# Optimization experiments

Measured on AMD Instinct MI355X. Metric: run time of the kernel, lower is better.

The kernel has to match this reference:

```python
import jax, jax.numpy as jnp
import numpy as np

N_CTX = 10  # conv_concat is 10*idf -> idf, so the module expects exactly 10 contexts


def setup_inputs() -> dict:
    key = jax.random.key(0)
    ks = jax.random.split(key, 7)
    B, idf, ih, iw = 32, 256, 32, 32
    cdf, L = 512, 128
    inp = {
        "input": jax.random.normal(ks[0], (B, idf, ih, iw), jnp.float32),
        "contexts": jax.random.normal(ks[1], (N_CTX, B, cdf, L), jnp.float32),
        "Wc": jax.random.normal(ks[2], (idf, cdf), jnp.float32) * 0.02,      # conv_context 1x1, no bias
        "Wcat": jax.random.normal(ks[3], (idf, N_CTX * idf), jnp.float32) * 0.02,  # conv_concat 1x1, no bias
        "Wb": jax.random.normal(ks[4], (idf,), jnp.float32) * 0.02,          # conv_b weight applied to ones -> bias
        "gamma": jnp.ones((idf,), jnp.float32),
        "beta": jnp.zeros((idf,), jnp.float32),
    }
    return inp


def reference(input, contexts, Wc, Wcat, Wb, gamma, beta):
    B, idf, ih, iw = input.shape
    Q = ih * iw
    # target: [B, Q, idf]
    targetT = jnp.transpose(input.reshape(B, idf, Q), (0, 2, 1))
    # project all 10 contexts at once: conv1x1(cdf->idf) == matmul over channel dim
    sourceT = jnp.einsum('dc,nbcl->nbdl', Wc, contexts)          # [N, B, idf, L]
    # attention weights: bmm(targetT, sourceT) then softmax over source dim
    w = jax.nn.softmax(jnp.einsum('bqd,nbdl->nbql', targetT, sourceT), axis=-1)  # [N,B,Q,L]
    attn = jnp.einsum('nbql,nbdl->nbqd', w, sourceT)             # [N, B, Q, idf]
    # torch.cat over last dim in loop order i=0..9 -> interleave as [B,Q,N*idf]
    cat = jnp.transpose(attn, (1, 2, 0, 3)).reshape(B, Q, N_CTX * idf)
    # conv_concat (1x1) over channels + conv_b(ones) bias
    x = jnp.einsum('ef,bqf->bqe', Wcat, cat) + Wb                # [B, Q, idf]
    x = jax.nn.relu(x) + targetT
    # LayerNorm over idf, eps=0, affine
    mu = jnp.mean(x, axis=-1, keepdims=True)
    var = jnp.mean(jnp.square(x - mu), axis=-1, keepdims=True)
    return (x - mu) / jnp.sqrt(var) * gamma + beta
```

## Files before the change

### kernel.cpp

```cpp
#include <hip/hip_runtime.h>
#include <cstdint>

typedef unsigned short u16;
typedef unsigned int   u32;
typedef __bf16 bf16x8 __attribute__((ext_vector_type(8)));
typedef float  f32x4  __attribute__((ext_vector_type(4)));

#define NCTX 10
#define BSZ  32
#define IDF  256
#define QSZ  1024
#define CDF  512
#define LSZ  128

__device__ __forceinline__ u16 f2bf(float f) {
    u32 u = __float_as_uint(f);
    u += 0x7FFFu + ((u >> 16) & 1u);
    return (u16)(u >> 16);
}
__device__ __forceinline__ float bf2f(u16 h) {
    return __uint_as_float(((u32)h) << 16);
}

union U4V { uint4 u; bf16x8 v; };

__device__ __forceinline__ bf16x8 ldg16(const u16* p) {
    U4V t; t.u = *(const uint4*)p; return t.v;
}
__device__ __forceinline__ bf16x8 lds16(const u16* p) {
    U4V t; t.u = *(const uint4*)p; return t.v;
}
__device__ __forceinline__ bf16x8 pack8(const float* f) {
    U4V t;
    t.u.x = (u32)f2bf(f[0]) | ((u32)f2bf(f[1]) << 16);
    t.u.y = (u32)f2bf(f[2]) | ((u32)f2bf(f[3]) << 16);
    t.u.z = (u32)f2bf(f[4]) | ((u32)f2bf(f[5]) << 16);
    t.u.w = (u32)f2bf(f[6]) | ((u32)f2bf(f[7]) << 16);
    return t.v;
}
__device__ __forceinline__ f32x4 mfma16(bf16x8 a, bf16x8 b, f32x4 c) {
    return __builtin_amdgcn_mfma_f32_16x16x32_bf16(a, b, c, 0, 0, 0);
}

__device__ __forceinline__ void gl_lds16(const u16* g, u16* l) {
    __builtin_amdgcn_global_load_lds(
        (__attribute__((address_space(1))) void*)(g),
        (__attribute__((address_space(3))) void*)(l), 16, 0, 0);
}

__device__ __forceinline__ void vm_wait8() {
    asm volatile("s_waitcnt vmcnt(8)" ::: "memory");
    __builtin_amdgcn_sched_barrier(0);
}
__device__ __forceinline__ void vm_wait4() {
    asm volatile("s_waitcnt vmcnt(4)" ::: "memory");
    __builtin_amdgcn_sched_barrier(0);
}
__device__ __forceinline__ void vm_wait2() {
    asm volatile("s_waitcnt vmcnt(2)" ::: "memory");
    __builtin_amdgcn_sched_barrier(0);
}
__device__ __forceinline__ void vm_wait0() {
    asm volatile("s_waitcnt vmcnt(0)" ::: "memory");
    __builtin_amdgcn_sched_barrier(0);
}
__device__ __forceinline__ void mid_bar()  {
    __builtin_amdgcn_s_barrier();
    asm volatile("" ::: "memory");
}
__device__ __forceinline__ void end_bar()  {
    asm volatile("" ::: "memory");
    __builtin_amdgcn_s_barrier();
    asm volatile("" ::: "memory");
}
__device__ __forceinline__ void lg_bar()   {
    asm volatile("s_waitcnt lgkmcnt(0)" ::: "memory");
    __builtin_amdgcn_sched_barrier(0);
    __builtin_amdgcn_s_barrier();
    asm volatile("" ::: "memory");
}

__device__ __forceinline__ int swz_cg(int L) {
    return (((L & 3) + ((L >> 3) & 3)) & 3) * 8;
}
__device__ __forceinline__ int swz_off(int row, int quad) {
    return row * 32 + ((quad - (row >> 1)) & 3) * 8;
}

__device__ __forceinline__ void stage_ph1(u16* buf, const u16* sttH, const u16* sttL,
                                          int c0, int w, int L) {
    const int rr = L >> 2, cg = swz_cg(L);
#pragma unroll
    for (int j = 0; j < 4; ++j) {
        const int c = 4 * w + j;
        const int hi = (c < 8);
        const int ch = hi ? c : c - 8;
        const u16* src = (hi ? sttH : sttL) + (long)(ch * 16 + rr) * IDF + c0 + cg;
        gl_lds16(src, buf + (hi ? 0 : 4096) + ch * 512);
    }
}

__device__ __forceinline__ void stage_256(u16* buf, const u16* gbase, int stride,
                                          int c0, int w, int L) {
    const int rr = L >> 2, cg = swz_cg(L);
#pragma unroll
    for (int j = 0; j < 4; ++j) {
        const int c = 4 * w + j;
        const u16* src = gbase + (long)(c * 16 + rr) * stride + c0 + cg;
        gl_lds16(src, buf + c * 512);
    }
}

__device__ __forceinline__ void stage_128(u16* buf, const u16* gbase, int stride,
                                          int c0, int w, int L) {
    const int rr = L >> 2, cg = swz_cg(L);
#pragma unroll
    for (int j = 0; j < 2; ++j) {
        const int c = 2 * w + j;
        const u16* src = gbase + (long)(c * 16 + rr) * stride + c0 + cg;
        gl_lds16(src, buf + c * 512);
    }
}

__global__ __launch_bounds__(256) void k1_prep(const float* __restrict__ Wc,
                                               const float* __restrict__ Wcat,
                                               const float* __restrict__ input,
                                               const float* __restrict__ ctx,
                                               u16* __restrict__ Wc_hi,
                                               u16* __restrict__ Wc_lo,
                                               u16* __restrict__ Wcat_bf,
                                               u16* __restrict__ T_hi,
                                               u16* __restrict__ T_lo,
                                               u16* __restrict__ ctxT) {
    __shared__ float ts[64][33];
    const int bid = blockIdx.x;
    const int tid = threadIdx.x;

    if (bid < 3072) {
        int i = bid * 256 + tid;
        if (i < IDF * CDF) {
            float f = Wc[i];
            u16 h = f2bf(f);
            Wc_hi[i] = h;
            Wc_lo[i] = f2bf(f - bf2f(h));
        } else {
            int j = i - IDF * CDF;
            Wcat_bf[j] = f2bf(Wcat[j]);
        }
        return;
    }
    if (bid < 3072 + 4096) {
        const int r = bid - 3072;
        const int qt = r & 31, dt = (r >> 5) & 3, b = r >> 7;
        {
            const int dl = tid >> 2, q0 = (tid & 3) * 8;
            const float* src = input + ((long)(b * IDF + dt * 64 + dl)) * QSZ + qt * 32 + q0;
            float4 v0 = *(const float4*)src;
            float4 v1 = *(const float4*)(src + 4);
            ts[dl][q0 + 0] = v0.x; ts[dl][q0 + 1] = v0.y;
            ts[dl][q0 + 2] = v0.z; ts[dl][q0 + 3] = v0.w;
            ts[dl][q0 + 4] = v1.x; ts[dl][q0 + 5] = v1.y;
            ts[dl][q0 + 6] = v1.z; ts[dl][q0 + 7] = v1.w;
        }
        __syncthreads();
        {
            const int ql = tid >> 3, d8 = (tid & 7) * 8;
            u16 hi[8], lo[8];
#pragma unroll
            for (int i = 0; i < 8; ++i) {
                float f = ts[d8 + i][ql];
                hi[i] = f2bf(f);
                lo[i] = f2bf(f - bf2f(hi[i]));
            }
            const long o = ((long)(b * QSZ + qt * 32 + ql)) * IDF + dt * 64 + d8;
            *(uint4*)(T_hi + o) = *(const uint4*)hi;
            *(uint4*)(T_lo + o) = *(const uint4*)lo;
        }
        return;
    }
    {
        const int r = bid - (3072 + 4096);
        const int lt = r & 3, ct = (r >> 2) & 7, nb = r >> 5;
        const long ib = (long)nb * CDF * LSZ;
        {
            const int cl = tid >> 2, l0 = (tid & 3) * 8;
            const float* src = ctx + ib + (long)(ct * 64 + cl) * LSZ + lt * 32 + l0;
            float4 v0 = *(const float4*)src;
            float4 v1 = *(const float4*)(src + 4);
            ts[cl][l0 + 0] = v0.x; ts[cl][l0 + 1] = v0.y;
            ts[cl][l0 + 2] = v0.z; ts[cl][l0 + 3] = v0.w;
            ts[cl][l0 + 4] = v1.x; ts[cl][l0 + 5] = v1.y;
            ts[cl][l0 + 6] = v1.z; ts[cl][l0 + 7] = v1.w;
        }
        __syncthreads();
        {
            const int ll = tid >> 3, c8 = (tid & 7) * 8;
            u16 o8[8];
#pragma unroll
            for (int i = 0; i < 8; ++i) o8[i] = f2bf(ts[c8 + i][ll]);
            const long ob = (long)nb * LSZ * CDF;
            *(uint4*)(ctxT + ob + (long)(lt * 32 + ll) * CDF + ct * 64 + c8) =
                *(const uint4*)o8;
        }
    }
}

__global__ __launch_bounds__(256, 2) void k2_src(const u16* __restrict__ Wc_hi,
                                                 const u16* __restrict__ Wc_lo,
                                                 const u16* __restrict__ ctxT,
                                                 u16* __restrict__ sTT_hi,
                                                 u16* __restrict__ sTT_lo,
                                                 u16* __restrict__ s_dl) {
    __shared__ u16 bounce[128 * 136];
    __shared__ __align__(16) u16 BST[2][4096];
    const int tid = threadIdx.x;
    const int L = tid & 63, w = tid >> 6;
    const int wd = w >> 1, wl = w & 1, lr = L & 15, quad = L >> 4;
    const int dbase = blockIdx.x * 128;
    const int nb = blockIdx.y;
    const u16* ctxb = ctxT + (long)nb * LSZ * CDF;

    const f32x4 vz = {0.f, 0.f, 0.f, 0.f};
    f32x4 acc[4][4];
#pragma unroll
    for (int m = 0; m < 4; ++m)
#pragma unroll
        for (int nn = 0; nn < 4; ++nn) acc[m][nn] = vz;

    stage_128(BST[0], ctxb, CDF, 0, w, L);

    for (int kc = 0; kc < 16; ++kc) {
        const int cur = kc & 1;
        const int c0 = kc * 32 + quad * 8;
        bf16x8 aH[4], aL[4];
#pragma unroll
        for (int m = 0; m < 4; ++m) {
            const int d = dbase + 64 * wd + 16 * m + lr;
            aH[m] = ldg16(Wc_hi + d * CDF + c0);
            aL[m] = ldg16(Wc_lo + d * CDF + c0);
        }
        asm volatile("" ::: "memory");
        if (kc < 15) {
            stage_128(BST[cur ^ 1], ctxb, CDF, (kc + 1) * 32, w, L);
            vm_wait2();
        } else {
            vm_wait0();
        }
        mid_bar();

        bf16x8 bb[4];
#pragma unroll
        for (int nn = 0; nn < 4; ++nn)
            bb[nn] = lds16(BST[cur] + swz_off(64 * wl + 16 * nn + lr, quad));
#pragma unroll
        for (int m = 0; m < 4; ++m)
#pragma unroll
            for (int nn = 0; nn < 4; ++nn) {
                acc[m][nn] = mfma16(aH[m], bb[nn], acc[m][nn]);
                acc[m][nn] = mfma16(aL[m], bb[nn], acc[m][nn]);
            }
        end_bar();
    }

#pragma unroll
    for (int m = 0; m < 4; ++m)
#pragma unroll
        for (int nn = 0; nn < 4; ++nn)
#pragma unroll
            for (int r = 0; r < 4; ++r) {
                const int d = 64 * wd + 16 * m + 4 * quad + r;
                const int l = 64 * wl + 16 * nn + lr;
                bounce[l * 136 + d] = f2bf(acc[m][nn][r]);
            }
    __syncthreads();
    for (int i = tid; i < 2048; i += 256) {
        const int l = i >> 4, g = (i & 15) * 8;
        *(uint4*)(sTT_hi + ((long)nb * LSZ + l) * IDF + dbase + g) =
            *(const uint4*)(bounce + l * 136 + g);
    }
    __syncthreads();
#pragma unroll
    for (int m = 0; m < 4; ++m)
#pragma unroll
        for (int nn = 0; nn < 4; ++nn)
#pragma unroll
            for (int r = 0; r < 4; ++r) {
                const int d = 64 * wd + 16 * m + 4 * quad + r;
                const int l = 64 * wl + 16 * nn + lr;
                float c = acc[m][nn][r];
                u16 h = f2bf(c);
                bounce[l * 136 + d] = f2bf(c - bf2f(h));
            }
    __syncthreads();
    for (int i = tid; i < 2048; i += 256) {
        const int l = i >> 4, g = (i & 15) * 8;
        *(uint4*)(sTT_lo + ((long)nb * LSZ + l) * IDF + dbase + g) =
            *(const uint4*)(bounce + l * 136 + g);
    }
    __syncthreads();
#pragma unroll
    for (int m = 0; m < 4; ++m)
#pragma unroll
        for (int nn = 0; nn < 4; ++nn)
#pragma unroll
            for (int r = 0; r < 4; ++r) {
                const int d = 64 * wd + 16 * m + 4 * quad + r;
                const int l = 64 * wl + 16 * nn + lr;
                bounce[d * 136 + l] = f2bf(acc[m][nn][r]);
            }
    __syncthreads();
    for (int i = tid; i < 2048; i += 256) {
        const int d = i >> 4, g = (i & 15) * 8;
        *(uint4*)(s_dl + ((long)nb * IDF + dbase + d) * LSZ + g) =
            *(const uint4*)(bounce + d * 136 + g);
    }
}

__global__ __launch_bounds__(256, 2) void k3_attn(
    const u16* __restrict__ T_hi, const u16* __restrict__ T_lo,
    const u16* __restrict__ sTT_hi, const u16* __restrict__ sTT_lo,
    const u16* __restrict__ s_dl, const u16* __restrict__ Wcat_bf,
    const float* __restrict__ Wb, const float* __restrict__ gam_p,
    const float* __restrict__ bet_p, float* __restrict__ out)
{
    __shared__ __align__(16) u16 ST[2][8192];
    __shared__ float S[64 * 132];
    __shared__ float redA[256];
    __shared__ float redB[256];
    u16* attnL = (u16*)S;

    const int tid = threadIdx.x;
    const int L = tid & 63, w = tid >> 6;
    const int wq = w >> 1, wh = w & 1, lr = L & 15, quad = L >> 4;
    const int b = blockIdx.x;
    const int bq = b * QSZ + blockIdx.y * 64;

    const f32x4 vz = {0.f, 0.f, 0.f, 0.f};
    f32x4 x_acc[2][8];
#pragma unroll
    for (int m = 0; m < 2; ++m)
#pragma unroll
        for (int nn = 0; nn < 8; ++nn) x_acc[m][nn] = vz;

    bf16x8 aHr[2][2], aLr[2][2];

#pragma unroll
    for (int m = 0; m < 2; ++m) {
        const int ro = (bq + 32 * wq + 16 * m + lr) * IDF + quad * 8;
        aHr[0][m] = ldg16(T_hi + ro);
        aLr[0][m] = ldg16(T_lo + ro);
    }
    asm volatile("" ::: "memory");
    stage_ph1(ST[0], sTT_hi + (long)b * (LSZ * IDF), sTT_lo + (long)b * (LSZ * IDF),
              0, w, L);

    for (int n = 0; n < NCTX; ++n) {
        const int nb = n * BSZ + b;
        const u16* sttH = sTT_hi + (long)nb * (LSZ * IDF);
        const u16* sttL = sTT_lo + (long)nb * (LSZ * IDF);
        const u16* sdl  = s_dl  + (long)nb * (IDF * LSZ);
        const u16* wcat = Wcat_bf + n * IDF;

        f32x4 s_acc[2][4];
#pragma unroll
        for (int m = 0; m < 2; ++m)
#pragma unroll
            for (int nn = 0; nn < 4; ++nn) s_acc[m][nn] = vz;

#pragma unroll
        for (int kc = 0; kc < 8; ++kc) {
            const int cur = kc & 1;
            if (kc < 7) {
                const int c1 = (kc + 1) * 32 + quad * 8;
#pragma unroll
                for (int m = 0; m < 2; ++m) {
                    const int ro = (bq + 32 * wq + 16 * m + lr) * IDF + c1;
                    aHr[(kc + 1) & 1][m] = ldg16(T_hi + ro);
                    aLr[(kc + 1) & 1][m] = ldg16(T_lo + ro);
                }
                asm volatile("" ::: "memory");
                stage_ph1(ST[cur ^ 1], sttH, sttL, (kc + 1) * 32, w, L);
                vm_wait8();
            } else {
                stage_256(ST[cur ^ 1], sdl, LSZ, 0, w, L);
                vm_wait4();
            }
            mid_bar();

            const u16* Bh = ST[cur];
            const u16* Bl = ST[cur] + 4096;
            bf16x8 bH[4], bL[4];
#pragma unroll
            for (int nn = 0; nn < 4; ++nn) {
                const int off = swz_off(64 * wh + 16 * nn + lr, quad);
                bH[nn] = lds16(Bh + off);
                bL[nn] = lds16(Bl + off);
            }
#pragma unroll
            for (int m = 0; m < 2; ++m)
#pragma unroll
                for (int nn = 0; nn < 4; ++nn) {
                    s_acc[m][nn] = mfma16(aHr[cur][m], bH[nn], s_acc[m][nn]);
                    s_acc[m][nn] = mfma16(aHr[cur][m], bL[nn], s_acc[m][nn]);
                    s_acc[m][nn] = mfma16(aLr[cur][m], bH[nn], s_acc[m][nn]);
                }
            end_bar();
        }

#pragma unroll
        for (int m = 0; m < 2; ++m)
#pragma unroll
            for (int nn = 0; nn < 4; ++nn)
#pragma unroll
                for (int r = 0; r < 4; ++r)
                    S[(32 * wq + 16 * m + 4 * quad + r) * 132 + 64 * wh + 16 * nn + lr] =
                        s_acc[m][nn][r];
        lg_bar();

        {
            const int row = tid >> 2, sg = (tid & 3) * 32;
            float* sp = S + row * 132 + sg;
            float mx = sp[0];
#pragma unroll
            for (int i = 1; i < 32; ++i) mx = fmaxf(mx, sp[i]);
            redA[row * 4 + (tid & 3)] = mx;
            lg_bar();
            const float rm = fmaxf(fmaxf(redA[row * 4], redA[row * 4 + 1]),
                                   fmaxf(redA[row * 4 + 2], redA[row * 4 + 3]));
            float sm = 0.f;
#pragma unroll
            for (int i = 0; i < 32; ++i) {
                float e = __expf(sp[i] - rm);
                sp[i] = e;
                sm += e;
            }
            redB[row * 4 + (tid & 3)] = sm;
            lg_bar();
        }

        f32x4 a_acc[2][8];
#pragma unroll
        for (int m = 0; m < 2; ++m)
#pragma unroll
            for (int nn = 0; nn < 8; ++nn) a_acc[m][nn] = vz;

        for (int kc = 0; kc < 4; ++kc) {
            const int cur = kc & 1;
            if (kc < 3) stage_256(ST[cur ^ 1], sdl, LSZ, (kc + 1) * 32, w, L);
            else        stage_256(ST[cur ^ 1], wcat, NCTX * IDF, 0, w, L);
            vm_wait4();
            mid_bar();

            const int l0 = kc * 32 + quad * 8;
            bf16x8 af[2];
#pragma unroll
            for (int m = 0; m < 2; ++m)
                af[m] = pack8(S + (32 * wq + 16 * m + lr) * 132 + l0);
            const u16* Bd = ST[cur];
#pragma unroll
            for (int nn = 0; nn < 8; ++nn) {
                const int off = swz_off(128 * wh + 16 * nn + lr, quad);
                bf16x8 bf = lds16(Bd + off);
#pragma unroll
                for (int m = 0; m < 2; ++m)
                    a_acc[m][nn] = mfma16(af[m], bf, a_acc[m][nn]);
            }
            end_bar();
        }

        float invr[2][4];
#pragma unroll
        for (int m = 0; m < 2; ++m)
#pragma unroll
            for (int r = 0; r < 4; ++r) {
                const int row = 32 * wq + 16 * m + 4 * quad + r;
                invr[m][r] = 1.0f / (redB[row * 4] + redB[row * 4 + 1] +
                                     redB[row * 4 + 2] + redB[row * 4 + 3]);
            }
#pragma unroll
        for (int m = 0; m < 2; ++m)
#pragma unroll
            for (int nn = 0; nn < 8; ++nn)
#pragma unroll
                for (int r = 0; r < 4; ++r) {
                    const int row = 32 * wq + 16 * m + 4 * quad + r;
                    const int col = 128 * wh + 16 * nn + lr;
                    attnL[row * 264 + col] = f2bf(a_acc[m][nn][r] * invr[m][r]);
                }
        lg_bar();

        for (int kc = 0; kc < 8; ++kc) {
            const int cur = kc & 1;
            if (kc < 7) {
                stage_256(ST[cur ^ 1], wcat, NCTX * IDF, (kc + 1) * 32, w, L);
                vm_wait4();
            } else if (n < NCTX - 1) {
#pragma unroll
                for (int m = 0; m < 2; ++m) {
                    const int ro = (bq + 32 * wq + 16 * m + lr) * IDF + quad * 8;
                    aHr[0][m] = ldg16(T_hi + ro);
                    aLr[0][m] = ldg16(T_lo + ro);
                }
                asm volatile("" ::: "memory");
                const u16* nH = sTT_hi + (long)((n + 1) * BSZ + b) * (LSZ * IDF);
                const u16* nL = sTT_lo + (long)((n + 1) * BSZ + b) * (LSZ * IDF);
                stage_ph1(ST[cur ^ 1], nH, nL, 0, w, L);
                vm_wait8();
            } else {
                vm_wait0();
            }
            mid_bar();

            const int d0 = kc * 32 + quad * 8;
            bf16x8 af[2];
#pragma unroll
            for (int m = 0; m < 2; ++m) {
                U4V t;
                t.u = *(const uint4*)(attnL + (32 * wq + 16 * m + lr) * 264 + d0);
                af[m] = t.v;
            }
            const u16* Wt = ST[cur];
#pragma unroll
            for (int nn = 0; nn < 8; ++nn) {
                const int off = swz_off(128 * wh + 16 * nn + lr, quad);
                bf16x8 bf = lds16(Wt + off);
#pragma unroll
                for (int m = 0; m < 2; ++m)
                    x_acc[m][nn] = mfma16(af[m], bf, x_acc[m][nn]);
            }
            end_bar();
        }
    }
    vm_wait0();

    float gv[8], bv[8], wv[8];
    int ec[8];
#pragma unroll
    for (int nn = 0; nn < 8; ++nn) {
        ec[nn] = 128 * wh + 16 * nn + lr;
        wv[nn] = Wb[ec[nn]];
        gv[nn] = gam_p[ec[nn]];
        bv[nn] = bet_p[ec[nn]];
    }
#pragma unroll
    for (int m = 0; m < 2; ++m)
#pragma unroll
        for (int r = 0; r < 4; ++r) {
            const int row = 32 * wq + 16 * m + 4 * quad + r;
            const u16* th = T_hi + (long)(bq + row) * IDF;
            const u16* tl = T_lo + (long)(bq + row) * IDF;
#pragma unroll
            for (int nn = 0; nn < 8; ++nn) {
                float resid = bf2f(th[ec[nn]]) + bf2f(tl[ec[nn]]);
                x_acc[m][nn][r] = fmaxf(x_acc[m][nn][r] + wv[nn], 0.f) + resid;
            }
        }
    float s1[2][4], s2[2][4];
#pragma unroll
    for (int m = 0; m < 2; ++m)
#pragma unroll
        for (int r = 0; r < 4; ++r) {
            float a = 0.f, q2 = 0.f;
#pragma unroll
            for (int nn = 0; nn < 8; ++nn) {
                float v = x_acc[m][nn][r];
                a += v;
                q2 += v * v;
            }
            s1[m][r] = a;
            s2[m][r] = q2;
        }
#pragma unroll
    for (int off = 1; off <= 8; off <<= 1)
#pragma unroll
        for (int m = 0; m < 2; ++m)
#pragma unroll
            for (int r = 0; r < 4; ++r) {
                s1[m][r] += __shfl_xor(s1[m][r], off);
                s2[m][r] += __shfl_xor(s2[m][r], off);
            }
    if (lr == 0) {
#pragma unroll
        for (int m = 0; m < 2; ++m)
#pragma unroll
            for (int r = 0; r < 4; ++r) {
                const int row = 32 * wq + 16 * m + 4 * quad + r;
                redA[row * 4 + wh * 2]     = s1[m][r];
                redA[row * 4 + wh * 2 + 1] = s2[m][r];
            }
    }
    __syncthreads();
#pragma unroll
    for (int m = 0; m < 2; ++m)
#pragma unroll
        for (int r = 0; r < 4; ++r) {
            const int row = 32 * wq + 16 * m + 4 * quad + r;
            const float S1 = redA[row * 4] + redA[row * 4 + 2];
            const float S2 = redA[row * 4 + 1] + redA[row * 4 + 3];
            const float mu = S1 * (1.f / 256.f);
            const float rs = rsqrtf(S2 * (1.f / 256.f) - mu * mu);
            float* op = out + (long)(bq + row) * IDF;
#pragma unroll
            for (int nn = 0; nn < 8; ++nn)
                op[ec[nn]] = (x_acc[m][nn][r] - mu) * rs * gv[nn] + bv[nn];
        }
}

extern "C" void kernel_launch(void* const* d_in, const int* in_sizes, int n_in,
                              void* d_out, int out_size, void* d_ws, size_t ws_size,
                              hipStream_t stream) {
    const float* input    = (const float*)d_in[0];
    const float* contexts = (const float*)d_in[1];
    const float* Wc       = (const float*)d_in[2];
    const float* Wcat     = (const float*)d_in[3];
    const float* Wb       = (const float*)d_in[4];
    const float* gamma    = (const float*)d_in[5];
    const float* beta     = (const float*)d_in[6];
    float* out = (float*)d_out;

    char* ws = (char*)d_ws;
    size_t off = 0;
    u16* Wc_hi   = (u16*)(ws + off); off += (size_t)IDF * CDF * 2;
    u16* Wc_lo   = (u16*)(ws + off); off += (size_t)IDF * CDF * 2;
    u16* Wcat_bf = (u16*)(ws + off); off += (size_t)IDF * NCTX * IDF * 2;
    u16* T_hi    = (u16*)(ws + off); off += (size_t)BSZ * QSZ * IDF * 2;
    u16* T_lo    = (u16*)(ws + off); off += (size_t)BSZ * QSZ * IDF * 2;
    u16* ctxT    = (u16*)(ws + off); off += (size_t)NCTX * BSZ * LSZ * CDF * 2;
    u16* sTT_hi  = (u16*)(ws + off); off += (size_t)NCTX * BSZ * LSZ * IDF * 2;
    u16* sTT_lo  = (u16*)(ws + off); off += (size_t)NCTX * BSZ * LSZ * IDF * 2;
    u16* s_dl    = (u16*)(ws + off); off += (size_t)NCTX * BSZ * IDF * LSZ * 2;
    (void)in_sizes; (void)n_in; (void)out_size; (void)ws_size;

    k1_prep<<<17408, 256, 0, stream>>>(Wc, Wcat, input, contexts,
                                       Wc_hi, Wc_lo, Wcat_bf, T_hi, T_lo, ctxT);
    k2_src<<<dim3(2, NCTX * BSZ), 256, 0, stream>>>(Wc_hi, Wc_lo, ctxT, sTT_hi, sTT_lo, s_dl);
    k3_attn<<<dim3(BSZ, QSZ / 64), 256, 0, stream>>>(T_hi, T_lo, sTT_hi, sTT_lo, s_dl,
                                                     Wcat_bf, Wb, gamma, beta, out);
}
```

Measured before the change: 504.8 us.

## Split k3_attn row tiles across eight waves with 512-thread blocks

The attention kernel goes from 4 to 8 waves per block, so each wave owns 16 query rows instead of 32. Staging helpers, wait counts and softmax/LayerNorm reductions are reworked for the wider block. The goal is more latency hiding and fewer registers per wave, with launch bounds asking for 4 blocks per CU. The trade-off is that each B-fragment loaded from LDS now feeds half as many MFMAs, and the tighter register budget may cause spills.

```diff
diff --git a/kernel.cpp b/kernel.cpp
--- a/kernel.cpp
+++ b/kernel.cpp
@@ -48,10 +48,6 @@
         (__attribute__((address_space(3))) void*)(l), 16, 0, 0);
 }
 
-__device__ __forceinline__ void vm_wait8() {
-    asm volatile("s_waitcnt vmcnt(8)" ::: "memory");
-    __builtin_amdgcn_sched_barrier(0);
-}
 __device__ __forceinline__ void vm_wait4() {
     asm volatile("s_waitcnt vmcnt(4)" ::: "memory");
     __builtin_amdgcn_sched_barrier(0);
@@ -87,12 +83,23 @@
     return row * 32 + ((quad - (row >> 1)) & 3) * 8;
 }
 
-__device__ __forceinline__ void stage_ph1(u16* buf, const u16* sttH, const u16* sttL,
-                                          int c0, int w, int L) {
+__device__ __forceinline__ void stage_128_w4(u16* buf, const u16* gbase, int stride,
+                                             int c0, int w, int L) {
     const int rr = L >> 2, cg = swz_cg(L);
 #pragma unroll
-    for (int j = 0; j < 4; ++j) {
-        const int c = 4 * w + j;
+    for (int j = 0; j < 2; ++j) {
+        const int c = 2 * w + j;
+        const u16* src = gbase + (long)(c * 16 + rr) * stride + c0 + cg;
+        gl_lds16(src, buf + c * 512);
+    }
+}
+
+__device__ __forceinline__ void stage_ph1_w8(u16* buf, const u16* sttH, const u16* sttL,
+                                             int c0, int w, int L) {
+    const int rr = L >> 2, cg = swz_cg(L);
+#pragma unroll
+    for (int j = 0; j < 2; ++j) {
+        const int c = 2 * w + j;
         const int hi = (c < 8);
         const int ch = hi ? c : c - 8;
         const u16* src = (hi ? sttH : sttL) + (long)(ch * 16 + rr) * IDF + c0 + cg;
@@ -100,19 +107,8 @@
     }
 }
 
-__device__ __forceinline__ void stage_256(u16* buf, const u16* gbase, int stride,
-                                          int c0, int w, int L) {
-    const int rr = L >> 2, cg = swz_cg(L);
-#pragma unroll
-    for (int j = 0; j < 4; ++j) {
-        const int c = 4 * w + j;
-        const u16* src = gbase + (long)(c * 16 + rr) * stride + c0 + cg;
-        gl_lds16(src, buf + c * 512);
-    }
-}
-
-__device__ __forceinline__ void stage_128(u16* buf, const u16* gbase, int stride,
-                                          int c0, int w, int L) {
+__device__ __forceinline__ void stage_256_w8(u16* buf, const u16* gbase, int stride,
+                                             int c0, int w, int L) {
     const int rr = L >> 2, cg = swz_cg(L);
 #pragma unroll
     for (int j = 0; j < 2; ++j) {
@@ -227,7 +223,7 @@
 #pragma unroll
         for (int nn = 0; nn < 4; ++nn) acc[m][nn] = vz;
 
-    stage_128(BST[0], ctxb, CDF, 0, w, L);
+    stage_128_w4(BST[0], ctxb, CDF, 0, w, L);
 
     for (int kc = 0; kc < 16; ++kc) {
         const int cur = kc & 1;
@@ -241,7 +237,7 @@
         }
         asm volatile("" ::: "memory");
         if (kc < 15) {
-            stage_128(BST[cur ^ 1], ctxb, CDF, (kc + 1) * 32, w, L);
+            stage_128_w4(BST[cur ^ 1], ctxb, CDF, (kc + 1) * 32, w, L);
             vm_wait2();
         } else {
             vm_wait0();
@@ -316,7 +312,7 @@
     }
 }
 
-__global__ __launch_bounds__(256, 2) void k3_attn(
+__global__ __launch_bounds__(512, 4) void k3_attn(
     const u16* __restrict__ T_hi, const u16* __restrict__ T_lo,
     const u16* __restrict__ sTT_hi, const u16* __restrict__ sTT_lo,
     const u16* __restrict__ s_dl, const u16* __restrict__ Wcat_bf,
@@ -325,34 +321,32 @@
 {
     __shared__ __align__(16) u16 ST[2][8192];
     __shared__ float S[64 * 132];
-    __shared__ float redA[256];
-    __shared__ float redB[256];
+    __shared__ float redA[512];
+    __shared__ float redB[512];
     u16* attnL = (u16*)S;
 
     const int tid = threadIdx.x;
     const int L = tid & 63, w = tid >> 6;
-    const int wq = w >> 1, wh = w & 1, lr = L & 15, quad = L >> 4;
+    const int wq = w >> 1, wh = w & 1;
+    const int lr = L & 15, quad = L >> 4;
     const int b = blockIdx.x;
     const int bq = b * QSZ + blockIdx.y * 64;
 
     const f32x4 vz = {0.f, 0.f, 0.f, 0.f};
-    f32x4 x_acc[2][8];
-#pragma unroll
-    for (int m = 0; m < 2; ++m)
-#pragma unroll
-        for (int nn = 0; nn < 8; ++nn) x_acc[m][nn] = vz;
-
-    bf16x8 aHr[2][2], aLr[2][2];
-
-#pragma unroll
-    for (int m = 0; m < 2; ++m) {
-        const int ro = (bq + 32 * wq + 16 * m + lr) * IDF + quad * 8;
-        aHr[0][m] = ldg16(T_hi + ro);
-        aLr[0][m] = ldg16(T_lo + ro);
+    f32x4 x_acc[8];
+#pragma unroll
+    for (int nn = 0; nn < 8; ++nn) x_acc[nn] = vz;
+
+    bf16x8 aHr[2], aLr[2];
+
+    {
+        const int ro = (bq + 16 * wq + lr) * IDF + quad * 8;
+        aHr[0] = ldg16(T_hi + ro);
+        aLr[0] = ldg16(T_lo + ro);
     }
     asm volatile("" ::: "memory");
-    stage_ph1(ST[0], sTT_hi + (long)b * (LSZ * IDF), sTT_lo + (long)b * (LSZ * IDF),
-              0, w, L);
+    stage_ph1_w8(ST[0], sTT_hi + (long)b * (LSZ * IDF), sTT_lo + (long)b * (LSZ * IDF),
+                 0, w, L);
 
     for (int n = 0; n < NCTX; ++n) {
         const int nb = n * BSZ + b;
@@ -361,29 +355,26 @@
         const u16* sdl  = s_dl  + (long)nb * (IDF * LSZ);
         const u16* wcat = Wcat_bf + n * IDF;
 
-        f32x4 s_acc[2][4];
-#pragma unroll
-        for (int m = 0; m < 2; ++m)
-#pragma unroll
-            for (int nn = 0; nn < 4; ++nn) s_acc[m][nn] = vz;
+        f32x4 s_acc[4];
+#pragma unroll
+        for (int nn = 0; nn < 4; ++nn) s_acc[nn] = vz;
 
 #pragma unroll
         for (int kc = 0; kc < 8; ++kc) {
             const int cur = kc & 1;
             if (kc < 7) {
                 const int c1 = (kc + 1) * 32 + quad * 8;
-#pragma unroll
-                for (int m = 0; m < 2; ++m) {
-                    const int ro = (bq + 32 * wq + 16 * m + lr) * IDF + c1;
-                    aHr[(kc + 1) & 1][m] = ldg16(T_hi + ro);
-                    aLr[(kc + 1) & 1][m] = ldg16(T_lo + ro);
+                {
+                    const int ro = (bq + 16 * wq + lr) * IDF + c1;
+                    aHr[(kc + 1) & 1] = ldg16(T_hi + ro);
+                    aLr[(kc + 1) & 1] = ldg16(T_lo + ro);
                 }
                 asm volatile("" ::: "memory");
-                stage_ph1(ST[cur ^ 1], sttH, sttL, (kc + 1) * 32, w, L);
-                vm_wait8();
+                stage_ph1_w8(ST[cur ^ 1], sttH, sttL, (kc + 1) * 32, w, L);
+                vm_wait4();
             } else {
-                stage_256(ST[cur ^ 1], sdl, LSZ, 0, w, L);
-                vm_wait4();
+                stage_256_w8(ST[cur ^ 1], sdl, LSZ, 0, w, L);
+                vm_wait2();
             }
             mid_bar();
 
@@ -397,136 +388,120 @@
                 bL[nn] = lds16(Bl + off);
             }
 #pragma unroll
-            for (int m = 0; m < 2; ++m)
-#pragma unroll
-                for (int nn = 0; nn < 4; ++nn) {
-                    s_acc[m][nn] = mfma16(aHr[cur][m], bH[nn], s_acc[m][nn]);
-                    s_acc[m][nn] = mfma16(aHr[cur][m], bL[nn], s_acc[m][nn]);
-                    s_acc[m][nn] = mfma16(aLr[cur][m], bH[nn], s_acc[m][nn]);
-                }
+            for (int nn = 0; nn < 4; ++nn) {
+                s_acc[nn] = mfma16(aHr[cur], bH[nn], s_acc[nn]);
+                s_acc[nn] = mfma16(aHr[cur], bL[nn], s_acc[nn]);
+                s_acc[nn] = mfma16(aLr[cur], bH[nn], s_acc[nn]);
+            }
             end_bar();
         }
 
 #pragma unroll
-        for (int m = 0; m < 2; ++m)
-#pragma unroll
-            for (int nn = 0; nn < 4; ++nn)
-#pragma unroll
-                for (int r = 0; r < 4; ++r)
-                    S[(32 * wq + 16 * m + 4 * quad + r) * 132 + 64 * wh + 16 * nn + lr] =
-                        s_acc[m][nn][r];
+        for (int nn = 0; nn < 4; ++nn)
+#pragma unroll
+            for (int r = 0; r < 4; ++r)
+                S[(16 * wq + 4 * quad + r) * 132 + 64 * wh + 16 * nn + lr] =
+                    s_acc[nn][r];
         lg_bar();
 
         {
-            const int row = tid >> 2, sg = (tid & 3) * 32;
+            const int row = tid >> 3, sg = (tid & 7) * 16;
             float* sp = S + row * 132 + sg;
             float mx = sp[0];
 #pragma unroll
-            for (int i = 1; i < 32; ++i) mx = fmaxf(mx, sp[i]);
-            redA[row * 4 + (tid & 3)] = mx;
+            for (int i = 1; i < 16; ++i) mx = fmaxf(mx, sp[i]);
+            redA[row * 8 + (tid & 7)] = mx;
             lg_bar();
-            const float rm = fmaxf(fmaxf(redA[row * 4], redA[row * 4 + 1]),
-                                   fmaxf(redA[row * 4 + 2], redA[row * 4 + 3]));
+            float rm = redA[row * 8];
+#pragma unroll
+            for (int j = 1; j < 8; ++j) rm = fmaxf(rm, redA[row * 8 + j]);
             float sm = 0.f;
 #pragma unroll
-            for (int i = 0; i < 32; ++i) {
+            for (int i = 0; i < 16; ++i) {
                 float e = __expf(sp[i] - rm);
                 sp[i] = e;
                 sm += e;
             }
-            redB[row * 4 + (tid & 3)] = sm;
+            redB[row * 8 + (tid & 7)] = sm;
             lg_bar();
         }
 
-        f32x4 a_acc[2][8];
-#pragma unroll
-        for (int m = 0; m < 2; ++m)
-#pragma unroll
-            for (int nn = 0; nn < 8; ++nn) a_acc[m][nn] = vz;
+        f32x4 a_acc[8];
+#pragma unroll
+        for (int nn = 0; nn < 8; ++nn) a_acc[nn] = vz;
 
         for (int kc = 0; kc < 4; ++kc) {
             const int cur = kc & 1;
-            if (kc < 3) stage_256(ST[cur ^ 1], sdl, LSZ, (kc + 1) * 32, w, L);
-            else        stage_256(ST[cur ^ 1], wcat, NCTX * IDF, 0, w, L);
-            vm_wait4();
+            if (kc < 3) stage_256_w8(ST[cur ^ 1], sdl, LSZ, (kc + 1) * 32, w, L);
+            else        stage_256_w8(ST[cur ^ 1], wcat, NCTX * IDF, 0, w, L);
+            vm_wait2();
             mid_bar();
 
             const int l0 = kc * 32 + quad * 8;
-            bf16x8 af[2];
-#pragma unroll
-            for (int m = 0; m < 2; ++m)
-                af[m] = pack8(S + (32 * wq + 16 * m + lr) * 132 + l0);
+            bf16x8 af = pack8(S + (16 * wq + lr) * 132 + l0);
             const u16* Bd = ST[cur];
 #pragma unroll
             for (int nn = 0; nn < 8; ++nn) {
                 const int off = swz_off(128 * wh + 16 * nn + lr, quad);
                 bf16x8 bf = lds16(Bd + off);
-#pragma unroll
-                for (int m = 0; m < 2; ++m)
-                    a_acc[m][nn] = mfma16(af[m], bf, a_acc[m][nn]);
+                a_acc[nn] = mfma16(af, bf, a_acc[nn]);
             }
             end_bar();
         }
 
-        float invr[2][4];
-#pragma unroll
-        for (int m = 0; m < 2; ++m)
+        float invr[4];
+#pragma unroll
+        for (int r = 0; r < 4; ++r) {
+            const int row = 16 * wq + 4 * quad + r;
+            float sm = redB[row * 8];
+#pragma unroll
+            for (int j = 1; j < 8; ++j) sm += redB[row * 8 + j];
+            invr[r] = 1.0f / sm;
+        }
+#pragma unroll
+        for (int nn = 0; nn < 8; ++nn)
 #pragma unroll
             for (int r = 0; r < 4; ++r) {
-                const int row = 32 * wq + 16 * m + 4 * quad + r;
-                invr[m][r] = 1.0f / (redB[row * 4] + redB[row * 4 + 1] +
-                                     redB[row * 4 + 2] + redB[row * 4 + 3]);
-            }
-#pragma unroll
-        for (int m = 0; m < 2; ++m)
-#pragma unroll
-            for (int nn = 0; nn < 8; ++nn)
-#pragma unroll
-                for (int r = 0; r < 4; ++r) {
-                    const int row = 32 * wq + 16 * m + 4 * quad + r;
-                    const int col = 128 * wh + 16 * nn + lr;
-                    attnL[row * 264 + col] = f2bf(a_acc[m][nn][r] * invr[m][r]);
-                }
+                const int row = 16 * wq + 4 * quad + r;
+                const int col = 128 * wh + 16 * nn + lr;
+                attnL[row * 264 + col] = f2bf(a_acc[nn][r] * invr[r]);
+            }
         lg_bar();
 
         for (int kc = 0; kc < 8; ++kc) {
             const int cur = kc & 1;
             if (kc < 7) {
-                stage_256(ST[cur ^ 1], wcat, NCTX * IDF, (kc + 1) * 32, w, L);
-                vm_wait4();
+                stage_256_w8(ST[cur ^ 1], wcat, NCTX * IDF, (kc + 1) * 32, w, L);
+                vm_wait2();
             } else if (n < NCTX - 1) {
-#pragma unroll
-                for (int m = 0; m < 2; ++m) {
-                    const int ro = (bq + 32 * wq + 16 * m + lr) * IDF + quad * 8;
-                    aHr[0][m] = ldg16(T_hi + ro);
-                    aLr[0][m] = ldg16(T_lo + ro);
+                {
+                    const int ro = (bq + 16 * wq + lr) * IDF + quad * 8;
+                    aHr[0] = ldg16(T_hi + ro);
+                    aLr[0] = ldg16(T_lo + ro);
                 }
                 asm volatile("" ::: "memory");
                 const u16* nH = sTT_hi + (long)((n + 1) * BSZ + b) * (LSZ * IDF);
                 const u16* nL = sTT_lo + (long)((n + 1) * BSZ + b) * (LSZ * IDF);
-                stage_ph1(ST[cur ^ 1], nH, nL, 0, w, L);
-                vm_wait8();
+                stage_ph1_w8(ST[cur ^ 1], nH, nL, 0, w, L);
+                vm_wait4();
             } else {
                 vm_wait0();
             }
             mid_bar();
 
             const int d0 = kc * 32 + quad * 8;
-            bf16x8 af[2];
-#pragma unroll
-            for (int m = 0; m < 2; ++m) {
+            bf16x8 af;
+            {
                 U4V t;
-                t.u = *(const uint4*)(attnL + (32 * wq + 16 * m + lr) * 264 + d0);
-                af[m] = t.v;
+                t.u = *(const uint4*)(attnL + (16 * wq + lr) * 264 + d0);
+                af = t.v;
             }
             const u16* Wt = ST[cur];
 #pragma unroll
             for (int nn = 0; nn < 8; ++nn) {
                 const int off = swz_off(128 * wh + 16 * nn + lr, quad);
                 bf16x8 bf = lds16(Wt + off);
-#pragma unroll
-                for (int m = 0; m < 2; ++m)
-                    x_acc[m][nn] = mfma16(af[m], bf, x_acc[m][nn]);
+                x_acc[nn] = mfma16(af, bf, x_acc[nn]);
             }
             end_bar();
         }
@@ -543,67 +518,57 @@
         bv[nn] = bet_p[ec[nn]];
     }
 #pragma unroll
-    for (int m = 0; m < 2; ++m)
+    for (int r = 0; r < 4; ++r) {
+        const int row = 16 * wq + 4 * quad + r;
+        const u16* th = T_hi + (long)(bq + row) * IDF;
+        const u16* tl = T_lo + (long)(bq + row) * IDF;
+#pragma unroll
+        for (int nn = 0; nn < 8; ++nn) {
+            float resid = bf2f(th[ec[nn]]) + bf2f(tl[ec[nn]]);
+            x_acc[nn][r] = fmaxf(x_acc[nn][r] + wv[nn], 0.f) + resid;
+        }
+    }
+    float s1[4], s2[4];
+#pragma unroll
+    for (int r = 0; r < 4; ++r) {
+        float a = 0.f, q2 = 0.f;
+#pragma unroll
+        for (int nn = 0; nn < 8; ++nn) {
+            float v = x_acc[nn][r];
+            a += v;
+            q2 += v * v;
+        }
+        s1[r] = a;
+        s2[r] = q2;
+    }
+#pragma unroll
+    for (int off = 1; off <= 8; off <<= 1)
 #pragma unroll
         for (int r = 0; r < 4; ++r) {
-            const int row = 32 * wq + 16 * m + 4 * quad + r;
-            const u16* th = T_hi + (long)(bq + row) * IDF;
-            const u16* tl = T_lo + (long)(bq + row) * IDF;
-#pragma unroll
-            for (int nn = 0; nn < 8; ++nn) {
-                float resid = bf2f(th[ec[nn]]) + bf2f(tl[ec[nn]]);
-                x_acc[m][nn][r] = fmaxf(x_acc[m][nn][r] + wv[nn], 0.f) + resid;
-            }
-        }
-    float s1[2][4], s2[2][4];
-#pragma unroll
-    for (int m = 0; m < 2; ++m)
+            s1[r] += __shfl_xor(s1[r], off);
+            s2[r] += __shfl_xor(s2[r], off);
+        }
+    if (lr == 0) {
 #pragma unroll
         for (int r = 0; r < 4; ++r) {
-            float a = 0.f, q2 = 0.f;
-#pragma unroll
-            for (int nn = 0; nn < 8; ++nn) {
-                float v = x_acc[m][nn][r];
-                a += v;
-                q2 += v * v;
-            }
-            s1[m][r] = a;
-            s2[m][r] = q2;
-        }
-#pragma unroll
-    for (int off = 1; off <= 8; off <<= 1)
-#pragma unroll
-        for (int m = 0; m < 2; ++m)
-#pragma unroll
-            for (int r = 0; r < 4; ++r) {
-                s1[m][r] += __shfl_xor(s1[m][r], off);
-                s2[m][r] += __shfl_xor(s2[m][r], off);
-            }
-    if (lr == 0) {
-#pragma unroll
-        for (int m = 0; m < 2; ++m)
-#pragma unroll
-            for (int r = 0; r < 4; ++r) {
-                const int row = 32 * wq + 16 * m + 4 * quad + r;
-                redA[row * 4 + wh * 2]     = s1[m][r];
-                redA[row * 4 + wh * 2 + 1] = s2[m][r];
-            }
+            const int row = 16 * wq + 4 * quad + r;
+            redA[row * 4 + wh * 2]     = s1[r];
+            redA[row * 4 + wh * 2 + 1] = s2[r];
+        }
     }
     __syncthreads();
 #pragma unroll
-    for (int m = 0; m < 2; ++m)
-#pragma unroll
-        for (int r = 0; r < 4; ++r) {
-            const int row = 32 * wq + 16 * m + 4 * quad + r;
-            const float S1 = redA[row * 4] + redA[row * 4 + 2];
-            const float S2 = redA[row * 4 + 1] + redA[row * 4 + 3];
-            const float mu = S1 * (1.f / 256.f);
-            const float rs = rsqrtf(S2 * (1.f / 256.f) - mu * mu);
-            float* op = out + (long)(bq + row) * IDF;
-#pragma unroll
-            for (int nn = 0; nn < 8; ++nn)
-                op[ec[nn]] = (x_acc[m][nn][r] - mu) * rs * gv[nn] + bv[nn];
-        }
+    for (int r = 0; r < 4; ++r) {
+        const int row = 16 * wq + 4 * quad + r;
+        const float S1 = redA[row * 4] + redA[row * 4 + 2];
+        const float S2 = redA[row * 4 + 1] + redA[row * 4 + 3];
+        const float mu = S1 * (1.f / 256.f);
+        const float rs = rsqrtf(S2 * (1.f / 256.f) - mu * mu);
+        float* op = out + (long)(bq + row) * IDF;
+#pragma unroll
+        for (int nn = 0; nn < 8; ++nn)
+            op[ec[nn]] = (x_acc[nn][r] - mu) * rs * gv[nn] + bv[nn];
+    }
 }
 
 extern "C" void kernel_launch(void* const* d_in, const int* in_sizes, int n_in,
@@ -634,6 +599,6 @@
     k1_prep<<<17408, 256, 0, stream>>>(Wc, Wcat, input, contexts,
                                        Wc_hi, Wc_lo, Wcat_bf, T_hi, T_lo, ctxT);
     k2_src<<<dim3(2, NCTX * BSZ), 256, 0, stream>>>(Wc_hi, Wc_lo, ctxT, sTT_hi, sTT_lo, s_dl);
-    k3_attn<<<dim3(BSZ, QSZ / 64), 256, 0, stream>>>(T_hi, T_lo, sTT_hi, sTT_lo, s_dl,
+    k3_attn<<<dim3(BSZ, QSZ / 64), 512, 0, stream>>>(T_hi, T_lo, sTT_hi, sTT_lo, s_dl,
                                                      Wcat_bf, Wb, gamma, beta, out);
 }
```

After: 483.0 us. 1.05x faster.
